# Optimization experiments

Hardware: AMD Instinct MI355X
Metric: run time of the kernel (lower is better)

Reference implementation:

```python
import jax, jax.numpy as jnp
import numpy as np

N_HEAD = 16
N_EMBD = 1024
B, T = 2, 2048


def setup_inputs() -> dict:
    key = jax.random.key(0)
    ks = jax.random.split(key, 5)
    C = N_EMBD
    x = jax.random.normal(ks[0], (B, T, C), dtype=jnp.float32)
    # nn.Linear default init scale ~ 1/sqrt(fan_in); use small normal for numerics
    s = 1.0 / np.sqrt(C)
    W_attn = jax.random.normal(ks[1], (C, 3 * C), dtype=jnp.float32) * s
    b_attn = jax.random.normal(ks[2], (3 * C,), dtype=jnp.float32) * s
    W_proj = jax.random.normal(ks[3], (C, C), dtype=jnp.float32) * s
    b_proj = jax.random.normal(ks[4], (C,), dtype=jnp.float32) * s
    return {"x": x, "W_attn": W_attn, "b_attn": b_attn, "W_proj": W_proj, "b_proj": b_proj}


def reference(x, W_attn, b_attn, W_proj, b_proj):
    Bs, Ts, C = x.shape
    H = N_HEAD
    D = C // H  # head dim
    qkv = x @ W_attn + b_attn  # [B, T, 3C]
    q, k, v = jnp.split(qkv, 3, axis=2)
    # [B, T, H, D] -> [B, H, T, D]
    q = q.reshape(Bs, Ts, H, D).transpose(0, 2, 1, 3)
    k = k.reshape(Bs, Ts, H, D).transpose(0, 2, 1, 3)
    v = v.reshape(Bs, Ts, H, D).transpose(0, 2, 1, 3)
    scale = 1.0 / jnp.sqrt(jnp.asarray(D, dtype=x.dtype))
    att = jnp.einsum("bhqd,bhkd->bhqk", q, k) * scale  # [B, H, T, T]
    causal = jnp.tril(jnp.ones((Ts, Ts), dtype=bool))
    att = jnp.where(causal, att, -jnp.inf)
    att = jax.nn.softmax(att, axis=-1)
    y = jnp.einsum("bhqk,bhkd->bhqd", att, v)  # [B, H, T, D]
    y = y.transpose(0, 2, 1, 3).reshape(Bs, Ts, C)
    return y @ W_proj + b_proj
```

## Files before the change

kernel.cpp:

```cpp
#include <hip/hip_runtime.h>
#include <stdint.h>

typedef unsigned short u16;
typedef __attribute__((ext_vector_type(8))) short bf16x8;
typedef __attribute__((ext_vector_type(4))) float f32x4;
typedef __attribute__((ext_vector_type(4))) int   i32x4;
typedef __attribute__((ext_vector_type(4))) unsigned short u16x4;

#define MFMA16(a, b, c) __builtin_amdgcn_mfma_f32_16x16x32_bf16((a), (b), (c), 0, 0, 0)

#define BATCH 2
#define TSEQ  2048
#define CEMB  1024
#define NHEAD 16
#define DHEAD 64
#define BHTOT 32
#define MROWS 4096

__device__ __forceinline__ u16 bf16r(float f) {
  uint32_t u = __builtin_bit_cast(uint32_t, f);
  u += 0x7fffu + ((u >> 16) & 1u);
  return (u16)(u >> 16);
}

__device__ __forceinline__ void gl2lds16(const void* g, void* l) {
  __builtin_amdgcn_global_load_lds(
      (const __attribute__((address_space(1))) uint32_t*)g,
      (__attribute__((address_space(3))) uint32_t*)l, 16, 0, 0);
}

__global__ void conv_x(const float* __restrict__ x, u16* __restrict__ xb, int n) {
  int i = (blockIdx.x * blockDim.x + threadIdx.x) * 4;
  if (i < n) {
    f32x4 v = *(const f32x4*)(x + i);
    u16x4 o;
    o[0] = bf16r(v[0]); o[1] = bf16r(v[1]); o[2] = bf16r(v[2]); o[3] = bf16r(v[3]);
    *(u16x4*)(xb + i) = o;
  }
}

__global__ void transpose_w(const float* __restrict__ W, u16* __restrict__ WT, int K, int N) {
  __shared__ float t[32][33];
  int k0 = blockIdx.y * 32, n0 = blockIdx.x * 32;
  int tx = threadIdx.x & 31, ty = threadIdx.x >> 5;
  for (int i = 0; i < 4; i++)
    t[ty + i * 8][tx] = W[(size_t)(k0 + ty + i * 8) * N + n0 + tx];
  __syncthreads();
  for (int i = 0; i < 4; i++)
    WT[(size_t)(n0 + ty + i * 8) * K + k0 + tx] = bf16r(t[tx][ty + i * 8]);
}

__device__ __forceinline__ void gemm_mainloop(const u16* __restrict__ A,
                                              const u16* __restrict__ Bt,
                                              int K, int m0, int n0,
                                              u16* AsU, u16* BsU, f32x4 acc[4][4]) {
  const int tid = threadIdx.x;
  const int wv = tid >> 6, ln = tid & 63;
  const int lr = ln & 15, lg = ln >> 4;
  const int wr = (wv >> 1) * 64, wc = (wv & 1) * 64;

  for (int mi = 0; mi < 4; mi++)
    for (int ni = 0; ni < 4; ni++) acc[mi][ni] = f32x4{0.f, 0.f, 0.f, 0.f};

  for (int k0 = 0; k0 < K; k0 += 32) {
    for (int p = 0; p < 2; ++p) {
      int chunk = p * 256 + tid;
      int row = chunk >> 2;
      int c8  = (chunk & 3) << 3;
      u16* abase = AsU + (size_t)(p * 256 + wv * 64) * 8;
      u16* bbase = BsU + (size_t)(p * 256 + wv * 64) * 8;
      gl2lds16(A  + (size_t)(m0 + row) * K + k0 + c8, abase);
      gl2lds16(Bt + (size_t)(n0 + row) * K + k0 + c8, bbase);
    }
    __syncthreads();
    bf16x8 af[4], bf[4];
    for (int mi = 0; mi < 4; mi++)
      af[mi] = *(const bf16x8*)&AsU[(size_t)(wr + mi * 16 + lr) * 32 + lg * 8];
    for (int ni = 0; ni < 4; ni++)
      bf[ni] = *(const bf16x8*)&BsU[(size_t)(wc + ni * 16 + lr) * 32 + lg * 8];
    for (int mi = 0; mi < 4; mi++)
      for (int ni = 0; ni < 4; ni++)
        acc[mi][ni] = MFMA16(af[mi], bf[ni], acc[mi][ni]);
    __syncthreads();
  }
}

__global__ __launch_bounds__(256, 2) void qkv_gemm(const u16* __restrict__ xb,
                                                   const u16* __restrict__ WaT,
                                                   const float* __restrict__ b_attn,
                                                   u16* __restrict__ qb, u16* __restrict__ kb,
                                                   u16* __restrict__ vT) {
  __shared__ u16 AsU[128 * 32];
  __shared__ u16 BsU[128 * 32];
  const int m0 = blockIdx.y * 128, n0 = blockIdx.x * 128;
  f32x4 acc[4][4];
  gemm_mainloop(xb, WaT, CEMB, m0, n0, AsU, BsU, acc);

  const int tid = threadIdx.x;
  const int wv = tid >> 6, ln = tid & 63, lr = ln & 15, lg = ln >> 4;
  const int wr = (wv >> 1) * 64, wc = (wv & 1) * 64;
  for (int mi = 0; mi < 4; mi++)
    for (int ni = 0; ni < 4; ni++) {
      int col = n0 + wc + ni * 16 + lr;
      float bias = b_attn[col];
      int which = col >> 10;
      int cl = col & 1023, h = cl >> 6, d = cl & 63;
      for (int j = 0; j < 4; j++) {
        int m = m0 + wr + mi * 16 + lg * 4 + j;
        int b = m >> 11, t = m & 2047;
        u16 bv = bf16r(acc[mi][ni][j] + bias);
        size_t bh = (size_t)(b * NHEAD + h);
        if (which == 0)      qb[(bh * TSEQ + t) * DHEAD + d] = bv;
        else if (which == 1) kb[(bh * TSEQ + t) * DHEAD + d] = bv;
        else                 vT[(bh * DHEAD + d) * TSEQ + t] = bv;
      }
    }
}

__global__ __launch_bounds__(256, 2) void attn(const u16* __restrict__ qb,
                                               const u16* __restrict__ kb,
                                               const u16* __restrict__ vT,
                                               u16* __restrict__ yb) {
  const int flat = blockIdx.x;
  const int myid = (flat & 7) * 64 + (flat >> 3);
  const int bh = myid >> 4, qblk = myid & 15;
  const int tid = threadIdx.x, wv = tid >> 6, ln = tid & 63, lr = ln & 15, lg = ln >> 4;

  __shared__ u16 Ks[64][72];
  __shared__ u16 Vs[64][72];
  __shared__ u16 Ps[4][2][16][72];

  const int wq0 = qblk * 128 + wv * 32;
  const float SCL = 0.125f * 1.44269504f;

  bf16x8 qf[2][2];
#pragma unroll
  for (int qs = 0; qs < 2; qs++) {
    const u16* qrow = qb + ((size_t)bh * TSEQ + (wq0 + qs * 16 + lr)) * DHEAD + lg * 8;
    qf[qs][0] = *(const bf16x8*)(qrow);
    qf[qs][1] = *(const bf16x8*)(qrow + 32);
  }

  f32x4 acc[2][4];
#pragma unroll
  for (int qs = 0; qs < 2; qs++)
#pragma unroll
    for (int df = 0; df < 4; df++) acc[qs][df] = f32x4{0.f, 0.f, 0.f, 0.f};
  float mrun[2] = {-1e30f, -1e30f}, lrun[2] = {0.f, 0.f};

  const int ntiles = 2 * qblk + 2;
  const int srow = tid >> 3, sc8 = (tid & 7) << 3;

  i32x4 kreg[2], vreg[2];
#pragma unroll
  for (int p = 0; p < 2; p++) {
    int row = p * 32 + srow;
    kreg[p] = *(const i32x4*)(kb + ((size_t)bh * TSEQ + row) * DHEAD + sc8);
    vreg[p] = *(const i32x4*)(vT + ((size_t)bh * DHEAD + row) * TSEQ + sc8);
  }

  for (int kt = 0; kt < ntiles; kt++) {
    const int kbase = kt * 64;
#pragma unroll
    for (int p = 0; p < 2; p++) {
      int row = p * 32 + srow;
      *(i32x4*)&Ks[row][sc8] = kreg[p];
      *(i32x4*)&Vs[row][sc8] = vreg[p];
    }
    __syncthreads();
    if (kt + 1 < ntiles) {
      const int nb = kbase + 64;
#pragma unroll
      for (int p = 0; p < 2; p++) {
        int row = p * 32 + srow;
        kreg[p] = *(const i32x4*)(kb + ((size_t)bh * TSEQ + nb + row) * DHEAD + sc8);
        vreg[p] = *(const i32x4*)(vT + ((size_t)bh * DHEAD + row) * TSEQ + nb + sc8);
      }
    }

    f32x4 s[2][4];
#pragma unroll
    for (int st = 0; st < 4; st++) {
      bf16x8 kf0 = *(const bf16x8*)&Ks[st * 16 + lr][lg * 8];
      bf16x8 kf1 = *(const bf16x8*)&Ks[st * 16 + lr][32 + lg * 8];
#pragma unroll
      for (int qs = 0; qs < 2; qs++) {
        f32x4 z = f32x4{0.f, 0.f, 0.f, 0.f};
        z = MFMA16(kf0, qf[qs][0], z);
        z = MFMA16(kf1, qf[qs][1], z);
        s[qs][st] = z;
      }
    }

#pragma unroll
    for (int qs = 0; qs < 2; qs++) {
      const int qg = wq0 + qs * 16 + lr;
      float mt = -1e30f;
#pragma unroll
      for (int st = 0; st < 4; st++)
#pragma unroll
        for (int j = 0; j < 4; j++) {
          int kg = kbase + st * 16 + lg * 4 + j;
          float v = (kg <= qg) ? s[qs][st][j] * SCL : -1e30f;
          s[qs][st][j] = v;
          mt = fmaxf(mt, v);
        }
      mt = fmaxf(mt, __shfl_xor(mt, 16));
      mt = fmaxf(mt, __shfl_xor(mt, 32));
      float mnew = fmaxf(mrun[qs], mt);
      float al = __builtin_amdgcn_exp2f(mrun[qs] - mnew);
      float rs = 0.f;
#pragma unroll
      for (int st = 0; st < 4; st++)
#pragma unroll
        for (int j = 0; j < 4; j++) {
          float p = __builtin_amdgcn_exp2f(s[qs][st][j] - mnew);
          s[qs][st][j] = p;
          rs += p;
        }
      rs += __shfl_xor(rs, 16);
      rs += __shfl_xor(rs, 32);
      lrun[qs] = lrun[qs] * al + rs;
      mrun[qs] = mnew;
#pragma unroll
      for (int df = 0; df < 4; df++)
#pragma unroll
        for (int j = 0; j < 4; j++) acc[qs][df][j] *= al;
#pragma unroll
      for (int st = 0; st < 4; st++) {
        uint32_t w0 = (uint32_t)bf16r(s[qs][st][0]) | ((uint32_t)bf16r(s[qs][st][1]) << 16);
        uint32_t w1 = (uint32_t)bf16r(s[qs][st][2]) | ((uint32_t)bf16r(s[qs][st][3]) << 16);
        *(uint32_t*)&Ps[wv][qs][lr][st * 16 + lg * 4]     = w0;
        *(uint32_t*)&Ps[wv][qs][lr][st * 16 + lg * 4 + 2] = w1;
      }
    }
    __asm__ volatile("s_waitcnt lgkmcnt(0)" ::: "memory");
    __builtin_amdgcn_sched_barrier(0);

    bf16x8 pf[2][2];
#pragma unroll
    for (int qs = 0; qs < 2; qs++)
#pragma unroll
      for (int ks = 0; ks < 2; ks++)
        pf[qs][ks] = *(const bf16x8*)&Ps[wv][qs][lr][ks * 32 + lg * 8];
#pragma unroll
    for (int df = 0; df < 4; df++)
#pragma unroll
      for (int ks = 0; ks < 2; ks++) {
        bf16x8 vf = *(const bf16x8*)&Vs[df * 16 + lr][ks * 32 + lg * 8];
        acc[0][df] = MFMA16(vf, pf[0][ks], acc[0][df]);
        acc[1][df] = MFMA16(vf, pf[1][ks], acc[1][df]);
      }
    __syncthreads();
  }

  const int b = bh >> 4, h = bh & 15;
#pragma unroll
  for (int qs = 0; qs < 2; qs++) {
    float inv = 1.f / lrun[qs];
    int tg = wq0 + qs * 16 + lr;
#pragma unroll
    for (int df = 0; df < 4; df++) {
      u16x4 o;
#pragma unroll
      for (int j = 0; j < 4; j++) o[j] = bf16r(acc[qs][df][j] * inv);
      *(u16x4*)&yb[((size_t)b * TSEQ + tg) * CEMB + h * 64 + df * 16 + lg * 4] = o;
    }
  }
}

__global__ __launch_bounds__(256, 2) void proj_gemm(const u16* __restrict__ yb,
                                                    const u16* __restrict__ WpT,
                                                    const float* __restrict__ b_proj,
                                                    float* __restrict__ out) {
  __shared__ u16 AsU[128 * 32];
  __shared__ u16 BsU[128 * 32];
  const int m0 = blockIdx.y * 128, n0 = blockIdx.x * 128;
  f32x4 acc[4][4];
  gemm_mainloop(yb, WpT, CEMB, m0, n0, AsU, BsU, acc);

  const int tid = threadIdx.x;
  const int wv = tid >> 6, ln = tid & 63, lr = ln & 15, lg = ln >> 4;
  const int wr = (wv >> 1) * 64, wc = (wv & 1) * 64;
  for (int mi = 0; mi < 4; mi++)
    for (int ni = 0; ni < 4; ni++) {
      int col = n0 + wc + ni * 16 + lr;
      float bias = b_proj[col];
      for (int j = 0; j < 4; j++) {
        int m = m0 + wr + mi * 16 + lg * 4 + j;
        out[(size_t)m * CEMB + col] = acc[mi][ni][j] + bias;
      }
    }
}

extern "C" void kernel_launch(void* const* d_in, const int* in_sizes, int n_in,
                              void* d_out, int out_size, void* d_ws, size_t ws_size,
                              hipStream_t stream) {
  const float* x      = (const float*)d_in[0];
  const float* W_attn = (const float*)d_in[1];
  const float* b_attn = (const float*)d_in[2];
  const float* W_proj = (const float*)d_in[3];
  const float* b_proj = (const float*)d_in[4];
  float* out = (float*)d_out;
  char* ws = (char*)d_ws;

  u16* xb  = (u16*)(ws);
  u16* WaT = (u16*)(ws + 8388608);
  u16* WpT = (u16*)(ws + 14680064);
  u16* qb  = (u16*)(ws + 16777216);
  u16* kb  = (u16*)(ws + 25165824);
  u16* vT  = (u16*)(ws + 33554432);
  u16* yb  = (u16*)(ws + 41943040);

  hipLaunchKernelGGL(conv_x, dim3(4096), dim3(256), 0, stream, x, xb, MROWS * CEMB);
  hipLaunchKernelGGL(transpose_w, dim3(96, 32), dim3(256), 0, stream, W_attn, WaT, 1024, 3072);
  hipLaunchKernelGGL(transpose_w, dim3(32, 32), dim3(256), 0, stream, W_proj, WpT, 1024, 1024);
  hipLaunchKernelGGL(qkv_gemm, dim3(24, 32), dim3(256), 0, stream, xb, WaT, b_attn, qb, kb, vT);
  hipLaunchKernelGGL(attn, dim3(512), dim3(256), 0, stream, qb, kb, vT, yb);
  hipLaunchKernelGGL(proj_gemm, dim3(8, 32), dim3(256), 0, stream, yb, WpT, b_proj, out);
}
```

Before: 226.2 us.

## Double-buffer K/V in attention, fold scale into Q, skip masking and rescale

The attention kernel now double-buffers K/V tiles in LDS, so each iteration needs one barrier instead of two, and the next tile's stores overlap compute. The softmax scale is folded into Q once at load, which adds an extra bf16 rounding of Q. Causal masking is skipped for tiles that lie fully below the diagonal, and the accumulator rescale is skipped when the running max does not grow. The block-to-work mapping is also reordered so heavy and light query blocks are interleaved across CUs for better load balance.

```diff
diff --git a/kernel.cpp b/kernel.cpp
--- a/kernel.cpp
+++ b/kernel.cpp
@@ -21,6 +21,17 @@
   uint32_t u = __builtin_bit_cast(uint32_t, f);
   u += 0x7fffu + ((u >> 16) & 1u);
   return (u16)(u >> 16);
+}
+
+__device__ __forceinline__ float bf2f(short v) {
+  return __builtin_bit_cast(float, ((uint32_t)(u16)v) << 16);
+}
+
+__device__ __forceinline__ bf16x8 scale8(bf16x8 a, float s) {
+  bf16x8 r;
+#pragma unroll
+  for (int i = 0; i < 8; i++) r[i] = (short)bf16r(bf2f(a[i]) * s);
+  return r;
 }
 
 __device__ __forceinline__ void gl2lds16(const void* g, void* l) {
@@ -122,12 +133,15 @@
                                                const u16* __restrict__ vT,
                                                u16* __restrict__ yb) {
   const int flat = blockIdx.x;
-  const int myid = (flat & 7) * 64 + (flat >> 3);
-  const int bh = myid >> 4, qblk = myid & 15;
+  const int x = flat & 7;
+  const int l = flat >> 3;
+  int bh, qblk;
+  if (l < 32) { bh = 4 * x + (l >> 3); qblk = 15 - (l & 7); }
+  else        { int l2 = l - 32; bh = 4 * x + (l2 >> 3); qblk = l2 & 7; }
   const int tid = threadIdx.x, wv = tid >> 6, ln = tid & 63, lr = ln & 15, lg = ln >> 4;
 
-  __shared__ u16 Ks[64][72];
-  __shared__ u16 Vs[64][72];
+  __shared__ u16 Ks[2][64][72];
+  __shared__ u16 Vs[2][64][72];
   __shared__ u16 Ps[4][2][16][72];
 
   const int wq0 = qblk * 128 + wv * 32;
@@ -137,8 +151,8 @@
 #pragma unroll
   for (int qs = 0; qs < 2; qs++) {
     const u16* qrow = qb + ((size_t)bh * TSEQ + (wq0 + qs * 16 + lr)) * DHEAD + lg * 8;
-    qf[qs][0] = *(const bf16x8*)(qrow);
-    qf[qs][1] = *(const bf16x8*)(qrow + 32);
+    qf[qs][0] = scale8(*(const bf16x8*)(qrow), SCL);
+    qf[qs][1] = scale8(*(const bf16x8*)(qrow + 32), SCL);
   }
 
   f32x4 acc[2][4];
@@ -155,34 +169,28 @@
 #pragma unroll
   for (int p = 0; p < 2; p++) {
     int row = p * 32 + srow;
-    kreg[p] = *(const i32x4*)(kb + ((size_t)bh * TSEQ + row) * DHEAD + sc8);
-    vreg[p] = *(const i32x4*)(vT + ((size_t)bh * DHEAD + row) * TSEQ + sc8);
-  }
-
+    i32x4 k0 = *(const i32x4*)(kb + ((size_t)bh * TSEQ + row) * DHEAD + sc8);
+    i32x4 v0 = *(const i32x4*)(vT + ((size_t)bh * DHEAD + row) * TSEQ + sc8);
+    *(i32x4*)&Ks[0][row][sc8] = k0;
+    *(i32x4*)&Vs[0][row][sc8] = v0;
+  }
+#pragma unroll
+  for (int p = 0; p < 2; p++) {
+    int row = p * 32 + srow;
+    kreg[p] = *(const i32x4*)(kb + ((size_t)bh * TSEQ + 64 + row) * DHEAD + sc8);
+    vreg[p] = *(const i32x4*)(vT + ((size_t)bh * DHEAD + row) * TSEQ + 64 + sc8);
+  }
+
+  int c = 0;
   for (int kt = 0; kt < ntiles; kt++) {
     const int kbase = kt * 64;
-#pragma unroll
-    for (int p = 0; p < 2; p++) {
-      int row = p * 32 + srow;
-      *(i32x4*)&Ks[row][sc8] = kreg[p];
-      *(i32x4*)&Vs[row][sc8] = vreg[p];
-    }
     __syncthreads();
-    if (kt + 1 < ntiles) {
-      const int nb = kbase + 64;
-#pragma unroll
-      for (int p = 0; p < 2; p++) {
-        int row = p * 32 + srow;
-        kreg[p] = *(const i32x4*)(kb + ((size_t)bh * TSEQ + nb + row) * DHEAD + sc8);
-        vreg[p] = *(const i32x4*)(vT + ((size_t)bh * DHEAD + row) * TSEQ + nb + sc8);
-      }
-    }
 
     f32x4 s[2][4];
 #pragma unroll
     for (int st = 0; st < 4; st++) {
-      bf16x8 kf0 = *(const bf16x8*)&Ks[st * 16 + lr][lg * 8];
-      bf16x8 kf1 = *(const bf16x8*)&Ks[st * 16 + lr][32 + lg * 8];
+      bf16x8 kf0 = *(const bf16x8*)&Ks[c][st * 16 + lr][lg * 8];
+      bf16x8 kf1 = *(const bf16x8*)&Ks[c][st * 16 + lr][32 + lg * 8];
 #pragma unroll
       for (int qs = 0; qs < 2; qs++) {
         f32x4 z = f32x4{0.f, 0.f, 0.f, 0.f};
@@ -192,40 +200,69 @@
       }
     }
 
+    if (kt + 1 < ntiles) {
+#pragma unroll
+      for (int p = 0; p < 2; p++) {
+        int row = p * 32 + srow;
+        *(i32x4*)&Ks[c ^ 1][row][sc8] = kreg[p];
+        *(i32x4*)&Vs[c ^ 1][row][sc8] = vreg[p];
+      }
+    }
+    if (kt + 2 < ntiles) {
+      const int nb = kbase + 128;
+#pragma unroll
+      for (int p = 0; p < 2; p++) {
+        int row = p * 32 + srow;
+        kreg[p] = *(const i32x4*)(kb + ((size_t)bh * TSEQ + nb + row) * DHEAD + sc8);
+        vreg[p] = *(const i32x4*)(vT + ((size_t)bh * DHEAD + row) * TSEQ + nb + sc8);
+      }
+    }
+
 #pragma unroll
     for (int qs = 0; qs < 2; qs++) {
-      const int qg = wq0 + qs * 16 + lr;
+      const int qgmin = wq0 + qs * 16;
       float mt = -1e30f;
-#pragma unroll
-      for (int st = 0; st < 4; st++)
-#pragma unroll
-        for (int j = 0; j < 4; j++) {
-          int kg = kbase + st * 16 + lg * 4 + j;
-          float v = (kg <= qg) ? s[qs][st][j] * SCL : -1e30f;
-          s[qs][st][j] = v;
-          mt = fmaxf(mt, v);
-        }
+      if (kbase + 63 <= qgmin) {
+#pragma unroll
+        for (int st = 0; st < 4; st++)
+#pragma unroll
+          for (int j = 0; j < 4; j++) mt = fmaxf(mt, s[qs][st][j]);
+      } else {
+        const int qg = qgmin + lr;
+#pragma unroll
+        for (int st = 0; st < 4; st++)
+#pragma unroll
+          for (int j = 0; j < 4; j++) {
+            int kg = kbase + st * 16 + lg * 4 + j;
+            float v = (kg <= qg) ? s[qs][st][j] : -1e30f;
+            s[qs][st][j] = v;
+            mt = fmaxf(mt, v);
+          }
+      }
       mt = fmaxf(mt, __shfl_xor(mt, 16));
       mt = fmaxf(mt, __shfl_xor(mt, 32));
-      float mnew = fmaxf(mrun[qs], mt);
-      float al = __builtin_amdgcn_exp2f(mrun[qs] - mnew);
+      if (!__all(mt <= mrun[qs])) {
+        float mnew = fmaxf(mrun[qs], mt);
+        float al = __builtin_amdgcn_exp2f(mrun[qs] - mnew);
+#pragma unroll
+        for (int df = 0; df < 4; df++)
+#pragma unroll
+          for (int j = 0; j < 4; j++) acc[qs][df][j] *= al;
+        lrun[qs] *= al;
+        mrun[qs] = mnew;
+      }
       float rs = 0.f;
 #pragma unroll
       for (int st = 0; st < 4; st++)
 #pragma unroll
         for (int j = 0; j < 4; j++) {
-          float p = __builtin_amdgcn_exp2f(s[qs][st][j] - mnew);
+          float p = __builtin_amdgcn_exp2f(s[qs][st][j] - mrun[qs]);
           s[qs][st][j] = p;
           rs += p;
         }
       rs += __shfl_xor(rs, 16);
       rs += __shfl_xor(rs, 32);
-      lrun[qs] = lrun[qs] * al + rs;
-      mrun[qs] = mnew;
-#pragma unroll
-      for (int df = 0; df < 4; df++)
-#pragma unroll
-        for (int j = 0; j < 4; j++) acc[qs][df][j] *= al;
+      lrun[qs] += rs;
 #pragma unroll
       for (int st = 0; st < 4; st++) {
         uint32_t w0 = (uint32_t)bf16r(s[qs][st][0]) | ((uint32_t)bf16r(s[qs][st][1]) << 16);
@@ -247,11 +284,11 @@
     for (int df = 0; df < 4; df++)
 #pragma unroll
       for (int ks = 0; ks < 2; ks++) {
-        bf16x8 vf = *(const bf16x8*)&Vs[df * 16 + lr][ks * 32 + lg * 8];
+        bf16x8 vf = *(const bf16x8*)&Vs[c][df * 16 + lr][ks * 32 + lg * 8];
         acc[0][df] = MFMA16(vf, pf[0][ks], acc[0][df]);
         acc[1][df] = MFMA16(vf, pf[1][ks], acc[1][df]);
       }
-    __syncthreads();
+    c ^= 1;
   }
 
   const int b = bh >> 4, h = bh & 15;
```

New measurement: 202.6 us. 10.4% less time.
